# Kernel tuning notes

Measured on AMD Instinct MI355X. Metric: run time of the kernel, lower is better.

Reference implementation:

```python
import jax, jax.numpy as jnp
import numpy as np

L, H, E, FF, B, S = 2, 8, 512, 2048, 8, 1024


def _layernorm(x, g, b, eps=1e-5):
    mu = jnp.mean(x, axis=-1, keepdims=True)
    var = jnp.mean(jnp.square(x - mu), axis=-1, keepdims=True)
    return (x - mu) * jax.lax.rsqrt(var + eps) * g + b


def setup_inputs() -> dict:
    key = jax.random.key(0)
    ks = jax.random.split(key, 16)
    sc = 1.0 / np.sqrt(E)
    d = {
        "x": jax.random.normal(ks[0], (B, S, E), jnp.float32),
        # per-layer, per-head disentangled projections: Linear(E,E) -> weight [out,in]
        "Wq": jax.random.normal(ks[1], (L, H, E, E), jnp.float32) * sc,
        "bq": jnp.zeros((L, H, E), jnp.float32),
        "Wk": jax.random.normal(ks[2], (L, H, E, E), jnp.float32) * sc,
        "bk": jnp.zeros((L, H, E), jnp.float32),
        "Wv": jax.random.normal(ks[3], (L, H, E, E), jnp.float32) * sc,
        "bv": jnp.zeros((L, H, E), jnp.float32),
        "Wo": jax.random.normal(ks[4], (L, H, E, E), jnp.float32) * sc,
        "bo": jnp.zeros((L, H, E), jnp.float32),
        "head_alphas": jax.random.uniform(ks[5], (H,), jnp.float32, 0.5, 1.5),
        "ln1_g": jnp.ones((L, E), jnp.float32),
        "ln1_b": jnp.zeros((L, E), jnp.float32),
        "W1": jax.random.normal(ks[6], (L, FF, E), jnp.float32) * sc,
        "b1": jnp.zeros((L, FF), jnp.float32),
        "W2": jax.random.normal(ks[7], (L, E, FF), jnp.float32) * (1.0 / np.sqrt(FF)),
        "b2": jnp.zeros((L, E), jnp.float32),
        "ln2_g": jnp.ones((L, E), jnp.float32),
        "ln2_b": jnp.zeros((L, E), jnp.float32),
    }
    return d


def reference(x, Wq, bq, Wk, bk, Wv, bv, Wo, bo, head_alphas,
              ln1_g, ln1_b, W1, b1, W2, b2, ln2_g, ln2_b):
    seq = x.shape[1]
    # causal additive mask, as generate_square_subsequent_mask
    causal = jnp.where(jnp.tril(jnp.ones((seq, seq), bool)), 0.0, -jnp.inf).astype(x.dtype)
    scale = jnp.sqrt(jnp.asarray(E, x.dtype))  # head_dim == embed_dim (disentangled)
    ha = head_alphas[None, :, None, None]
    for i in range(L):
        # disentangled per-head projections, batched over heads: [B,H,S,E]
        rq = jnp.einsum('bse,hoe->bhso', x, Wq[i]) + bq[i][None, :, None, :]
        rk = jnp.einsum('bse,hoe->bhso', x, Wk[i]) + bk[i][None, :, None, :]
        rv = jnp.einsum('bse,hoe->bhso', x, Wv[i]) + bv[i][None, :, None, :]
        scores = jnp.einsum('bhqd,bhkd->bhqk', rq, rk) / scale + causal
        attn = jax.nn.softmax(scores, axis=-1)
        ao = jnp.einsum('bhqk,bhkd->bhqd', attn, rv) * ha
        # per-head out_proj then sum over heads
        attn_out = jnp.einsum('bhsd,hod->bso', ao, Wo[i]) + jnp.sum(bo[i], axis=0)
        x = _layernorm(x + attn_out, ln1_g[i], ln1_b[i])
        h = jax.nn.relu(jnp.einsum('bse,fe->bsf', x, W1[i]) + b1[i])
        ff = jnp.einsum('bsf,ef->bse', h, W2[i]) + b2[i]
        x = _layernorm(x + ff, ln2_g[i], ln2_b[i])
    return x
```

## Files before the change

### kernel.cpp

```cpp
#include <hip/hip_runtime.h>
#include <hip/hip_bf16.h>
#include <stdint.h>

#define LL 2
#define HH 8
#define EE 512
#define FFD 2048
#define BB 8
#define SS 1024
#define CB 2
#define NCH (BB / CB)
#define PAIRS (CB * HH)

typedef unsigned short u16;
typedef __attribute__((ext_vector_type(8))) short bf16x8;
typedef __attribute__((ext_vector_type(4))) float f32x4;
typedef __attribute__((ext_vector_type(4))) int int4v;
typedef __attribute__((ext_vector_type(2))) int int2v;

__device__ __forceinline__ u16 f2bf(float f){
  union { float f; unsigned u; } c; c.f = f;
  unsigned r = (c.u + 0x7FFFu + ((c.u >> 16) & 1u)) >> 16;
  return (u16)r;
}

struct GP {
  const u16* A; const u16* B;
  const float* bias; const float* resid;
  void* out;
  long AsMHi, AsMLo, AsH;
  long BsNHi, BsNLo, BsH;
  long Abatch, Bbatch, Obatch, BiasB;
  long OsMHi, OsMLo, OsNHi, OsNLo;
  int M, N, K, causal, Kpart;
  float scale;
};

__device__ __forceinline__ int xcd_swz(int bid, int nwg){
  if (nwg < 16) return bid;
  const int q = nwg >> 3, r = nwg & 7;
  const int xcd = bid & 7, loc = bid >> 3;
  return (xcd < r ? xcd * (q + 1) : r * (q + 1) + (xcd - r) * q) + loc;
}

template<int EP>
__global__ __launch_bounds__(256, 3) void k_gemm(GP p){
  const int tilesN = p.N >> 7;
  const int bid = xcd_swz(blockIdx.x, gridDim.x);
  const int m0 = (bid / tilesN) << 7;
  const int n0 = (bid % tilesN) << 7;
  if (EP == 0 && p.causal && n0 > m0) return;
  const long bb = blockIdx.y;
  const u16* __restrict__ Ag = p.A + bb * p.Abatch;
  const u16* __restrict__ Bg = p.B + bb * p.Bbatch;

  __shared__ __align__(16) u16 As[128 * 64];
  __shared__ __align__(16) u16 Bs[128 * 64];
  char* AsB = (char*)As;
  char* BsB = (char*)Bs;

  const int t = threadIdx.x;
  const int lane = t & 63;
  const int wv = t >> 6;
  const int wr = (wv >> 1) << 6;
  const int wc = (wv & 1) << 6;

  long aoff[4], boff[4];
  #pragma unroll
  for (int j = 0; j < 4; ++j){
    const int r = ((wv << 2) + j) * 8 + (lane >> 3);
    const int kx = ((lane & 7) << 3) ^ ((r & 7) << 3);
    const int gm = m0 + r;
    aoff[j] = (long)(gm >> 10) * p.AsMHi + (long)(gm & 1023) * p.AsMLo + kx;
    const int gn = n0 + r;
    boff[j] = (long)(gn >> 9) * p.BsNHi + (long)(gn & 511) * p.BsNLo + kx;
  }

  int kBeg = 0;
  int Klim = p.K;
  if (EP == 2 && p.causal) { int kl = m0 + 128; Klim = kl < p.K ? kl : p.K; }
  if (EP == 5) { kBeg = (int)bb * p.Kpart; Klim = kBeg + p.Kpart; }

  f32x4 acc[4][4];
  #pragma unroll
  for (int a = 0; a < 4; ++a)
    #pragma unroll
    for (int b = 0; b < 4; ++b)
      acc[a][b] = (f32x4){0.f, 0.f, 0.f, 0.f};

  for (int k0 = kBeg; k0 < Klim; k0 += 64){
    const long ka = (long)(k0 >> 9) * p.AsH + (k0 & 511);
    const long kb = (long)(k0 >> 9) * p.BsH + (k0 & 511);
    __syncthreads();
    #pragma unroll
    for (int j = 0; j < 4; ++j){
      const int ldsOff = (((wv << 2) + j) << 9);
      __builtin_amdgcn_global_load_lds(
          (const __attribute__((address_space(1))) void*)(Ag + aoff[j] + ka),
          (__attribute__((address_space(3))) void*)(As + ldsOff), 16, 0, 0);
      __builtin_amdgcn_global_load_lds(
          (const __attribute__((address_space(1))) void*)(Bg + boff[j] + kb),
          (__attribute__((address_space(3))) void*)(Bs + ldsOff), 16, 0, 0);
    }
    __syncthreads();
    #pragma unroll
    for (int kk = 0; kk < 2; ++kk){
      bf16x8 af[4], bv[4];
      #pragma unroll
      for (int mi = 0; mi < 4; ++mi){
        int row = wr + (mi << 4) + (lane & 15);
        int bc = ((kk << 6) + ((lane >> 4) << 4)) ^ ((row & 7) << 4);
        af[mi] = *reinterpret_cast<const bf16x8*>(AsB + row * 128 + bc);
      }
      #pragma unroll
      for (int ni = 0; ni < 4; ++ni){
        int row = wc + (ni << 4) + (lane & 15);
        int bc = ((kk << 6) + ((lane >> 4) << 4)) ^ ((row & 7) << 4);
        bv[ni] = *reinterpret_cast<const bf16x8*>(BsB + row * 128 + bc);
      }
      #pragma unroll
      for (int mi = 0; mi < 4; ++mi)
        #pragma unroll
        for (int ni = 0; ni < 4; ++ni)
          acc[mi][ni] = __builtin_amdgcn_mfma_f32_16x16x32_bf16(af[mi], bv[ni], acc[mi][ni], 0, 0, 0);
    }
  }

  const int cm = (lane >> 4) << 2;
  const int cn = lane & 15;
  float biasv[4];
  if (EP == 1 || EP == 4){
    #pragma unroll
    for (int ni = 0; ni < 4; ++ni)
      biasv[ni] = p.bias[bb * p.BiasB + n0 + wc + (ni << 4) + cn];
  }
  #pragma unroll
  for (int mi = 0; mi < 4; ++mi){
    #pragma unroll
    for (int i = 0; i < 4; ++i){
      const int m = m0 + wr + (mi << 4) + cm + i;
      const long ob = bb * p.Obatch + (long)(m >> 10) * p.OsMHi + (long)(m & 1023) * p.OsMLo;
      #pragma unroll
      for (int ni = 0; ni < 4; ++ni){
        const int n = n0 + wc + (ni << 4) + cn;
        const long oa = ob + (long)(n >> 9) * p.OsNHi + (long)(n & 511) * p.OsNLo;
        float v = acc[mi][ni][i];
        if (EP == 0) ((u16*)p.out)[oa] = f2bf(v * p.scale);
        else if (EP == 1) ((u16*)p.out)[oa] = f2bf(v + biasv[ni]);
        else if (EP == 2) ((u16*)p.out)[oa] = f2bf(v);
        else if (EP == 5) ((float*)p.out)[oa] = v;
        else { float r = v + biasv[ni]; ((u16*)p.out)[oa] = f2bf(r > 0.f ? r : 0.f); }
      }
    }
  }
}

__global__ __launch_bounds__(128) void k_redln(const float* __restrict__ part,
                                               const float* __restrict__ bias,
                                               const float* __restrict__ resid,
                                               const float* __restrict__ g,
                                               const float* __restrict__ b,
                                               float* __restrict__ fdst,
                                               u16* __restrict__ bdst){
  const long row = blockIdx.x;
  const int t = threadIdx.x;
  const int col = t << 2;
  const long off = row * EE + col;
  const long nX = (long)BB * SS * EE;
  f32x4 s = *reinterpret_cast<const f32x4*>(part + off);
  #pragma unroll
  for (int q = 1; q < 4; ++q){
    f32x4 v = *reinterpret_cast<const f32x4*>(part + q * nX + off);
    s.x += v.x; s.y += v.y; s.z += v.z; s.w += v.w;
  }
  f32x4 bv = *reinterpret_cast<const f32x4*>(bias + col);
  f32x4 rv = *reinterpret_cast<const f32x4*>(resid + off);
  s.x += bv.x + rv.x; s.y += bv.y + rv.y; s.z += bv.z + rv.z; s.w += bv.w + rv.w;

  float ps = s.x + s.y + s.z + s.w;
  #pragma unroll
  for (int o = 32; o; o >>= 1) ps += __shfl_xor(ps, o);
  __shared__ float red[2], red2[2];
  if ((t & 63) == 0) red[t >> 6] = ps;
  __syncthreads();
  const float mean = (red[0] + red[1]) * (1.0f / EE);
  f32x4 d = { s.x - mean, s.y - mean, s.z - mean, s.w - mean };
  float pv = d.x * d.x + d.y * d.y + d.z * d.z + d.w * d.w;
  #pragma unroll
  for (int o = 32; o; o >>= 1) pv += __shfl_xor(pv, o);
  if ((t & 63) == 0) red2[t >> 6] = pv;
  __syncthreads();
  const float var = (red2[0] + red2[1]) * (1.0f / EE);
  const float rstd = rsqrtf(var + 1e-5f);
  f32x4 gv = *reinterpret_cast<const f32x4*>(g + col);
  f32x4 bb = *reinterpret_cast<const f32x4*>(b + col);
  f32x4 o4 = { d.x * rstd * gv.x + bb.x, d.y * rstd * gv.y + bb.y,
               d.z * rstd * gv.z + bb.z, d.w * rstd * gv.w + bb.w };
  *reinterpret_cast<f32x4*>(fdst + off) = o4;
  union { u16 us[4]; int2v v; } u;
  u.us[0] = f2bf(o4.x); u.us[1] = f2bf(o4.y);
  u.us[2] = f2bf(o4.z); u.us[3] = f2bf(o4.w);
  *reinterpret_cast<int2v*>(bdst + off) = u.v;
}

struct SetupP {
  const float *x, *Wq, *Wk, *Wv, *Wo, *W1, *W2, *bq, *bk, *bv, *bo;
  float *xf, *catb, *bos;
  u16 *xb, *wdst;
};
#define SETUP_TA 524288u
#define SETUP_TB 2621440u
#define SETUP_TC 25600u
__global__ __launch_bounds__(256) void k_setup(SetupP sp){
  const unsigned t = blockIdx.x * 256 + threadIdx.x;
  if (t < SETUP_TA){
    const int i = (int)t << 3;
    f32x4 a = *reinterpret_cast<const f32x4*>(sp.x + i);
    f32x4 b = *reinterpret_cast<const f32x4*>(sp.x + i + 4);
    *reinterpret_cast<f32x4*>(sp.xf + i) = a;
    *reinterpret_cast<f32x4*>(sp.xf + i + 4) = b;
    union { u16 us[8]; int4v v; } u;
    #pragma unroll
    for (int j = 0; j < 4; ++j){ u.us[j] = f2bf(a[j]); u.us[4 + j] = f2bf(b[j]); }
    *reinterpret_cast<int4v*>(sp.xb + i) = u.v;
  } else if (t < SETUP_TA + SETUP_TB){
    const size_t j = ((size_t)(t - SETUP_TA)) << 3;
    const size_t R = (size_t)4194304;
    const size_t F = (size_t)2097152;
    const float* src;
    size_t loc;
    if      (j < R)         { src = sp.Wq; loc = j; }
    else if (j < 2*R)       { src = sp.Wk; loc = j - R; }
    else if (j < 3*R)       { src = sp.Wv; loc = j - 2*R; }
    else if (j < 4*R)       { src = sp.Wo; loc = j - 3*R; }
    else if (j < 4*R + F)   { src = sp.W1; loc = j - 4*R; }
    else                    { src = sp.W2; loc = j - 4*R - F; }
    f32x4 a = *reinterpret_cast<const f32x4*>(src + loc);
    f32x4 b = *reinterpret_cast<const f32x4*>(src + loc + 4);
    union { u16 us[8]; int4v v; } u;
    #pragma unroll
    for (int q = 0; q < 4; ++q){ u.us[q] = f2bf(a[q]); u.us[4 + q] = f2bf(b[q]); }
    *reinterpret_cast<int4v*>(sp.wdst + j) = u.v;
  } else {
    const int j = (int)(t - SETUP_TA - SETUP_TB);
    if (j >= 2 * 12800) return;
    const int L = j / 12800;
    const int r = j - L * 12800;
    const int lw = L * HH * EE;
    float* catL = sp.catb + (size_t)L * 3 * HH * EE;
    if (r < 4096) catL[r] = sp.bq[lw + r];
    else if (r < 8192) catL[r] = sp.bk[lw + r - 4096];
    else if (r < 12288) catL[r] = sp.bv[lw + r - 8192];
    else {
      const int o = r - 12288;
      float s = 0.f;
      #pragma unroll
      for (int h = 0; h < HH; ++h) s += sp.bo[lw + h * EE + o];
      sp.bos[L * EE + o] = s;
    }
  }
}

__global__ __launch_bounds__(256) void k_softmax(u16* __restrict__ sp,
                                                 const float* __restrict__ alphas){
  const int wv = threadIdx.x >> 6;
  const long row = (long)blockIdx.x * 4 + wv;
  const int lane = threadIdx.x & 63;
  const int q = (int)(row & (SS - 1));
  const int h = (int)(row >> 10) & (HH - 1);
  const bool half2 = q >= 512;
  u16* rp = sp + row * SS;
  const int i0 = lane << 3;
  float v[8], v2[8];
  float lm = -1e30f;
  {
    bf16x8 a = *reinterpret_cast<const bf16x8*>(rp + i0);
    #pragma unroll
    for (int j = 0; j < 8; ++j){
      union { unsigned u; float f; } c; c.u = ((unsigned)(u16)a[j]) << 16;
      v[j] = (i0 + j <= q) ? c.f : -1e30f;
      lm = fmaxf(lm, v[j]);
    }
  }
  if (half2){
    bf16x8 a = *reinterpret_cast<const bf16x8*>(rp + i0 + 512);
    #pragma unroll
    for (int j = 0; j < 8; ++j){
      union { unsigned u; float f; } c; c.u = ((unsigned)(u16)a[j]) << 16;
      v2[j] = (i0 + 512 + j <= q) ? c.f : -1e30f;
      lm = fmaxf(lm, v2[j]);
    }
  }
  #pragma unroll
  for (int o = 32; o; o >>= 1) lm = fmaxf(lm, __shfl_xor(lm, o));
  float ls = 0.f;
  #pragma unroll
  for (int j = 0; j < 8; ++j){
    float e = exp2f((v[j] - lm) * 1.4426950408889634f);
    e = (i0 + j <= q) ? e : 0.f;
    v[j] = e; ls += e;
  }
  if (half2){
    #pragma unroll
    for (int j = 0; j < 8; ++j){
      float e = exp2f((v2[j] - lm) * 1.4426950408889634f);
      e = (i0 + 512 + j <= q) ? e : 0.f;
      v2[j] = e; ls += e;
    }
  }
  #pragma unroll
  for (int o = 32; o; o >>= 1) ls += __shfl_xor(ls, o);
  const float inv = alphas[h] / ls;
  {
    union { u16 us[8]; bf16x8 v8; } o8;
    #pragma unroll
    for (int j = 0; j < 8; ++j) o8.us[j] = f2bf(v[j] * inv);
    *reinterpret_cast<bf16x8*>(rp + i0) = o8.v8;
  }
  if (half2){
    union { u16 us[8]; bf16x8 v8; } o8;
    #pragma unroll
    for (int j = 0; j < 8; ++j) o8.us[j] = f2bf(v2[j] * inv);
    *reinterpret_cast<bf16x8*>(rp + i0 + 512) = o8.v8;
  }
}

__global__ __launch_bounds__(256) void k_transpose(const u16* __restrict__ v,
                                                   u16* __restrict__ vt){
  const long bh = blockIdx.y;
  const int ts = blockIdx.x >> 3;
  const int td = blockIdx.x & 7;
  const u16* src = v + bh * (long)(SS * EE) + (long)(ts * 64) * EE + td * 64;
  u16* dst = vt + bh * (long)(SS * EE) + (long)(td * 64) * SS + ts * 64;
  __shared__ __align__(16) u16 tl[64][80];
  const int t = threadIdx.x;
  #pragma unroll
  for (int it = 0; it < 2; ++it){
    int id = t + it * 256;
    int r = id >> 3, c = (id & 7) << 3;
    *reinterpret_cast<int4v*>(&tl[r][c]) =
        *reinterpret_cast<const int4v*>(src + (long)r * EE + c);
  }
  __syncthreads();
  #pragma unroll
  for (int it = 0; it < 2; ++it){
    int id = t + it * 256;
    int r = id >> 3, c = (id & 7) << 3;
    union { u16 us[8]; int4v v; } u;
    #pragma unroll
    for (int j = 0; j < 8; ++j) u.us[j] = tl[c + j][r];
    *reinterpret_cast<int4v*>(dst + (long)r * SS + c) = u.v;
  }
}

static inline void gemm_launch(int EP, const GP& p, int batch, hipStream_t st){
  dim3 g((unsigned)((p.M >> 7) * (p.N >> 7)), (unsigned)batch);
  switch (EP){
    case 0: k_gemm<0><<<g, 256, 0, st>>>(p); break;
    case 1: k_gemm<1><<<g, 256, 0, st>>>(p); break;
    case 2: k_gemm<2><<<g, 256, 0, st>>>(p); break;
    case 4: k_gemm<4><<<g, 256, 0, st>>>(p); break;
    case 5: k_gemm<5><<<g, 256, 0, st>>>(p); break;
  }
}

extern "C" void kernel_launch(void* const* d_in, const int* in_sizes, int n_in,
                              void* d_out, int out_size, void* d_ws, size_t ws_size,
                              hipStream_t stream){
  const float* x    = (const float*)d_in[0];
  const float* Wq   = (const float*)d_in[1];
  const float* bq   = (const float*)d_in[2];
  const float* Wk   = (const float*)d_in[3];
  const float* bk   = (const float*)d_in[4];
  const float* Wv   = (const float*)d_in[5];
  const float* bv   = (const float*)d_in[6];
  const float* Wo   = (const float*)d_in[7];
  const float* bo   = (const float*)d_in[8];
  const float* alph = (const float*)d_in[9];
  const float* ln1g = (const float*)d_in[10];
  const float* ln1b = (const float*)d_in[11];
  const float* W1   = (const float*)d_in[12];
  const float* b1   = (const float*)d_in[13];
  const float* W2   = (const float*)d_in[14];
  const float* b2   = (const float*)d_in[15];
  const float* ln2g = (const float*)d_in[16];
  const float* ln2b = (const float*)d_in[17];
  float* out = (float*)d_out;

  const size_t nWh = (size_t)HH * EE * EE;
  const size_t nWf = (size_t)FFD * EE;
  const size_t nX  = (size_t)BB * SS * EE;
  const size_t nQ  = (size_t)BB * HH * SS * EE;
  const size_t nChQ = (size_t)CB * HH * SS * EE;
  const size_t nScC = (size_t)PAIRS * SS * SS;

  char* w = (char*)d_ws;
  size_t off = 0;
  auto take = [&](size_t bytes) -> char* {
    char* p = w + off;
    off += (bytes + 255) & ~(size_t)255;
    return p;
  };

  u16* wqb = (u16*)take(4 * nWh);
  u16* wkb = (u16*)take(4 * nWh);
  u16* wvb = (u16*)take(4 * nWh);
  u16* wob = (u16*)take(4 * nWh);
  u16* w1b = (u16*)take(4 * nWf);
  u16* w2b = (u16*)take(4 * nWf);
  float* xf = (float*)take(4 * nX);
  u16* xb   = (u16*)take(2 * nX);
  u16* ao   = (u16*)take(2 * nQ);
  u16* qc   = (u16*)take(2 * nChQ);
  u16* kc   = (u16*)take(2 * nChQ);
  u16* vc   = (u16*)take(2 * nChQ);
  u16* vtc  = (u16*)take(2 * nChQ);
  u16* sc   = (u16*)take(2 * nScC);
  float* bo_sum  = (float*)take(4 * 2 * EE);
  float* qkvbias = (float*)take(4 * 2 * 3 * HH * EE);
  float* parts = (float*)qc;
  u16* hid = sc;

  SetupP spp{ x, Wq, Wk, Wv, Wo, W1, W2, bq, bk, bv, bo,
              xf, qkvbias, bo_sum, xb, wqb };
  k_setup<<<dim3((SETUP_TA + SETUP_TB + SETUP_TC) / 256), 256, 0, stream>>>(spp);

  for (int i = 0; i < LL; ++i){
    for (int c = 0; c < NCH; ++c){
      GP p{};
      p.AsMHi = (long)1024 * EE; p.AsMLo = EE; p.AsH = 0;
      p.BsNHi = (long)EE * EE;   p.BsNLo = EE; p.BsH = 0;
      p.Abatch = 0; p.Bbatch = (long)(2 * nWh); p.Obatch = (long)nChQ;
      p.BiasB = (long)HH * EE;
      p.OsMHi = (long)HH * SS * EE; p.OsMLo = EE;
      p.OsNHi = (long)SS * EE; p.OsNLo = 1;
      p.M = CB * SS; p.N = HH * EE; p.K = EE;
      p.A = xb + (size_t)c * CB * SS * EE;
      p.B = wqb + (size_t)i * nWh;
      p.bias = qkvbias + (size_t)i * 3 * HH * EE;
      p.out = qc; p.scale = 1.f; p.causal = 0; p.resid = nullptr; p.Kpart = 0;
      gemm_launch(1, p, 3, stream);

      k_transpose<<<dim3(128, PAIRS), 256, 0, stream>>>(vc, vtc);

      GP ps{};
      ps.A = qc; ps.B = kc; ps.out = sc;
      ps.AsMHi = 0; ps.AsMLo = EE; ps.AsH = 0;
      ps.BsNHi = (long)512 * EE; ps.BsNLo = EE; ps.BsH = 0;
      ps.Abatch = (long)SS * EE; ps.Bbatch = (long)SS * EE;
      ps.Obatch = (long)SS * SS; ps.BiasB = 0;
      ps.OsMHi = 0; ps.OsMLo = SS; ps.OsNHi = 512; ps.OsNLo = 1;
      ps.M = SS; ps.N = SS; ps.K = EE;
      ps.scale = 0.044194173824159216f; ps.causal = 1;
      ps.bias = nullptr; ps.resid = nullptr; ps.Kpart = 0;
      gemm_launch(0, ps, PAIRS, stream);

      k_softmax<<<dim3(PAIRS * SS / 4), 256, 0, stream>>>(sc, alph);

      GP pv{};
      pv.A = sc; pv.B = vtc; pv.out = ao + (size_t)c * nChQ;
      pv.AsMHi = 0; pv.AsMLo = SS; pv.AsH = 512;
      pv.BsNHi = 0; pv.BsNLo = SS; pv.BsH = 512;
      pv.Abatch = (long)SS * SS; pv.Bbatch = (long)EE * SS;
      pv.Obatch = (long)SS * EE; pv.BiasB = 0;
      pv.OsMHi = 0; pv.OsMLo = EE; pv.OsNHi = 0; pv.OsNLo = 1;
      pv.M = SS; pv.N = EE; pv.K = SS; pv.causal = 1;
      pv.scale = 1.f; pv.bias = nullptr; pv.resid = nullptr; pv.Kpart = 0;
      gemm_launch(2, pv, PAIRS, stream);
    }

    GP pw{};
    pw.A = ao; pw.B = wob + (size_t)i * nWh; pw.out = parts;
    pw.AsMHi = (long)HH * SS * EE; pw.AsMLo = EE; pw.AsH = (long)SS * EE;
    pw.BsNHi = 0; pw.BsNLo = EE; pw.BsH = (long)EE * EE;
    pw.Abatch = pw.Bbatch = 0; pw.Obatch = (long)nX; pw.BiasB = 0;
    pw.OsMHi = (long)1024 * EE; pw.OsMLo = EE; pw.OsNHi = 0; pw.OsNLo = 1;
    pw.M = BB * SS; pw.N = EE; pw.K = HH * EE; pw.Kpart = (HH * EE) / 4;
    pw.bias = nullptr; pw.resid = nullptr; pw.scale = 1.f; pw.causal = 0;
    gemm_launch(5, pw, 4, stream);
    k_redln<<<dim3(BB * SS), 128, 0, stream>>>(parts, bo_sum + (size_t)i * EE, xf,
                                               ln1g + (size_t)i * EE,
                                               ln1b + (size_t)i * EE, xf, xb);

    GP p1{};
    p1.A = xb; p1.B = w1b + (size_t)i * nWf; p1.out = hid;
    p1.AsMHi = (long)1024 * EE; p1.AsMLo = EE; p1.AsH = 0;
    p1.BsNHi = (long)512 * EE; p1.BsNLo = EE; p1.BsH = 0;
    p1.Abatch = p1.Bbatch = p1.Obatch = 0; p1.BiasB = 0;
    p1.OsMHi = (long)1024 * FFD; p1.OsMLo = FFD; p1.OsNHi = 512; p1.OsNLo = 1;
    p1.M = BB * SS; p1.N = FFD; p1.K = EE;
    p1.bias = b1 + (size_t)i * FFD; p1.resid = nullptr; p1.scale = 1.f;
    p1.causal = 0; p1.Kpart = 0;
    gemm_launch(4, p1, 1, stream);

    GP p2{};
    p2.A = hid; p2.B = w2b + (size_t)i * nWf; p2.out = parts;
    p2.AsMHi = (long)1024 * FFD; p2.AsMLo = FFD; p2.AsH = 512;
    p2.BsNHi = 0; p2.BsNLo = FFD; p2.BsH = 512;
    p2.Abatch = p2.Bbatch = 0; p2.Obatch = (long)nX; p2.BiasB = 0;
    p2.OsMHi = (long)1024 * EE; p2.OsMLo = EE; p2.OsNHi = 0; p2.OsNLo = 1;
    p2.M = BB * SS; p2.N = EE; p2.K = FFD; p2.Kpart = FFD / 4;
    p2.bias = nullptr; p2.resid = nullptr; p2.scale = 1.f; p2.causal = 0;
    gemm_launch(5, p2, 4, stream);
    float* fdst = (i == LL - 1) ? out : xf;
    k_redln<<<dim3(BB * SS), 128, 0, stream>>>(parts, b2 + (size_t)i * EE, xf,
                                               ln2g + (size_t)i * EE,
                                               ln2b + (size_t)i * EE, fdst, xb);
  }
}
```

Before: 1.229 ms.

## Fuse softmax with V transpose, chunk out-projection and LN1, enlarge batch chunks

Softmax and the V transpose become one kernel launch that splits work by block index. The per-head output projection, its split-K reduction and the first layernorm now run inside the batch-chunk loop, writing attention output back into the V buffer, so the full-size attention-output buffer is gone. The batch chunk grows from 2 to 4 sequences. Weight conversion to bf16 moves out of setup into a per-layer kernel, which halves the weight workspace. The aim is fewer launches, a smaller memory footprint and better cache locality, at the cost of more buffer aliasing that must stay correct.

```diff
diff --git a/kernel.cpp b/kernel.cpp
--- a/kernel.cpp
+++ b/kernel.cpp
@@ -8,7 +8,7 @@
 #define FFD 2048
 #define BB 8
 #define SS 1024
-#define CB 2
+#define CB 4
 #define NCH (BB / CB)
 #define PAIRS (CB * HH)
 
@@ -161,16 +161,18 @@
                                                const float* __restrict__ g,
                                                const float* __restrict__ b,
                                                float* __restrict__ fdst,
-                                               u16* __restrict__ bdst){
-  const long row = blockIdx.x;
+                                               u16* __restrict__ bdst,
+                                               long rowBase, long mn){
+  const long lrow = blockIdx.x;
+  const long row = rowBase + lrow;
   const int t = threadIdx.x;
   const int col = t << 2;
+  const long poff = lrow * EE + col;
   const long off = row * EE + col;
-  const long nX = (long)BB * SS * EE;
-  f32x4 s = *reinterpret_cast<const f32x4*>(part + off);
+  f32x4 s = *reinterpret_cast<const f32x4*>(part + poff);
   #pragma unroll
   for (int q = 1; q < 4; ++q){
-    f32x4 v = *reinterpret_cast<const f32x4*>(part + q * nX + off);
+    f32x4 v = *reinterpret_cast<const f32x4*>(part + q * mn + poff);
     s.x += v.x; s.y += v.y; s.z += v.z; s.w += v.w;
   }
   f32x4 bv = *reinterpret_cast<const f32x4*>(bias + col);
@@ -204,12 +206,11 @@
 }
 
 struct SetupP {
-  const float *x, *Wq, *Wk, *Wv, *Wo, *W1, *W2, *bq, *bk, *bv, *bo;
+  const float *x, *bq, *bk, *bv, *bo;
   float *xf, *catb, *bos;
-  u16 *xb, *wdst;
+  u16 *xb;
 };
 #define SETUP_TA 524288u
-#define SETUP_TB 2621440u
 #define SETUP_TC 25600u
 __global__ __launch_bounds__(256) void k_setup(SetupP sp){
   const unsigned t = blockIdx.x * 256 + threadIdx.x;
@@ -223,26 +224,8 @@
     #pragma unroll
     for (int j = 0; j < 4; ++j){ u.us[j] = f2bf(a[j]); u.us[4 + j] = f2bf(b[j]); }
     *reinterpret_cast<int4v*>(sp.xb + i) = u.v;
-  } else if (t < SETUP_TA + SETUP_TB){
-    const size_t j = ((size_t)(t - SETUP_TA)) << 3;
-    const size_t R = (size_t)4194304;
-    const size_t F = (size_t)2097152;
-    const float* src;
-    size_t loc;
-    if      (j < R)         { src = sp.Wq; loc = j; }
-    else if (j < 2*R)       { src = sp.Wk; loc = j - R; }
-    else if (j < 3*R)       { src = sp.Wv; loc = j - 2*R; }
-    else if (j < 4*R)       { src = sp.Wo; loc = j - 3*R; }
-    else if (j < 4*R + F)   { src = sp.W1; loc = j - 4*R; }
-    else                    { src = sp.W2; loc = j - 4*R - F; }
-    f32x4 a = *reinterpret_cast<const f32x4*>(src + loc);
-    f32x4 b = *reinterpret_cast<const f32x4*>(src + loc + 4);
-    union { u16 us[8]; int4v v; } u;
-    #pragma unroll
-    for (int q = 0; q < 4; ++q){ u.us[q] = f2bf(a[q]); u.us[4 + q] = f2bf(b[q]); }
-    *reinterpret_cast<int4v*>(sp.wdst + j) = u.v;
   } else {
-    const int j = (int)(t - SETUP_TA - SETUP_TB);
+    const int j = (int)(t - SETUP_TA);
     if (j >= 2 * 12800) return;
     const int L = j / 12800;
     const int r = j - L * 12800;
@@ -261,95 +244,122 @@
   }
 }
 
-__global__ __launch_bounds__(256) void k_softmax(u16* __restrict__ sp,
-                                                 const float* __restrict__ alphas){
-  const int wv = threadIdx.x >> 6;
-  const long row = (long)blockIdx.x * 4 + wv;
-  const int lane = threadIdx.x & 63;
-  const int q = (int)(row & (SS - 1));
-  const int h = (int)(row >> 10) & (HH - 1);
-  const bool half2 = q >= 512;
-  u16* rp = sp + row * SS;
-  const int i0 = lane << 3;
-  float v[8], v2[8];
-  float lm = -1e30f;
-  {
-    bf16x8 a = *reinterpret_cast<const bf16x8*>(rp + i0);
+struct WcvtP { const float *Wq, *Wk, *Wv, *Wo, *W1, *W2; u16* wdst; };
+#define WCVT_T 1310720u
+__global__ __launch_bounds__(256) void k_wcvt(WcvtP wp){
+  const unsigned t = blockIdx.x * 256 + threadIdx.x;
+  if (t >= WCVT_T) return;
+  const size_t j = ((size_t)t) << 3;
+  const size_t R = (size_t)2097152;
+  const size_t F = (size_t)1048576;
+  const float* src; size_t loc;
+  if      (j < R)       { src = wp.Wq; loc = j; }
+  else if (j < 2*R)     { src = wp.Wk; loc = j - R; }
+  else if (j < 3*R)     { src = wp.Wv; loc = j - 2*R; }
+  else if (j < 4*R)     { src = wp.Wo; loc = j - 3*R; }
+  else if (j < 4*R + F) { src = wp.W1; loc = j - 4*R; }
+  else                  { src = wp.W2; loc = j - 4*R - F; }
+  f32x4 a = *reinterpret_cast<const f32x4*>(src + loc);
+  f32x4 b = *reinterpret_cast<const f32x4*>(src + loc + 4);
+  union { u16 us[8]; int4v v; } u;
+  #pragma unroll
+  for (int q = 0; q < 4; ++q){ u.us[q] = f2bf(a[q]); u.us[4 + q] = f2bf(b[q]); }
+  *reinterpret_cast<int4v*>(wp.wdst + j) = u.v;
+}
+
+#define SM_BLOCKS (PAIRS * SS / 4)
+__global__ __launch_bounds__(256) void k_smt(u16* __restrict__ sp,
+                                             const float* __restrict__ alphas,
+                                             const u16* __restrict__ v,
+                                             u16* __restrict__ vt){
+  if (blockIdx.x < SM_BLOCKS){
+    const int wv = threadIdx.x >> 6;
+    const long row = (long)blockIdx.x * 4 + wv;
+    const int lane = threadIdx.x & 63;
+    const int q = (int)(row & (SS - 1));
+    const int h = (int)(row >> 10) & (HH - 1);
+    const bool half2 = q >= 512;
+    u16* rp = sp + row * SS;
+    const int i0 = lane << 3;
+    float vv[8], v2[8];
+    float lm = -1e30f;
+    {
+      bf16x8 a = *reinterpret_cast<const bf16x8*>(rp + i0);
+      #pragma unroll
+      for (int j = 0; j < 8; ++j){
+        union { unsigned u; float f; } c; c.u = ((unsigned)(u16)a[j]) << 16;
+        vv[j] = (i0 + j <= q) ? c.f : -1e30f;
+        lm = fmaxf(lm, vv[j]);
+      }
+    }
+    if (half2){
+      bf16x8 a = *reinterpret_cast<const bf16x8*>(rp + i0 + 512);
+      #pragma unroll
+      for (int j = 0; j < 8; ++j){
+        union { unsigned u; float f; } c; c.u = ((unsigned)(u16)a[j]) << 16;
+        v2[j] = (i0 + 512 + j <= q) ? c.f : -1e30f;
+        lm = fmaxf(lm, v2[j]);
+      }
+    }
+    #pragma unroll
+    for (int o = 32; o; o >>= 1) lm = fmaxf(lm, __shfl_xor(lm, o));
+    float ls = 0.f;
     #pragma unroll
     for (int j = 0; j < 8; ++j){
-      union { unsigned u; float f; } c; c.u = ((unsigned)(u16)a[j]) << 16;
-      v[j] = (i0 + j <= q) ? c.f : -1e30f;
-      lm = fmaxf(lm, v[j]);
-    }
-  }
-  if (half2){
-    bf16x8 a = *reinterpret_cast<const bf16x8*>(rp + i0 + 512);
-    #pragma unroll
-    for (int j = 0; j < 8; ++j){
-      union { unsigned u; float f; } c; c.u = ((unsigned)(u16)a[j]) << 16;
-      v2[j] = (i0 + 512 + j <= q) ? c.f : -1e30f;
-      lm = fmaxf(lm, v2[j]);
-    }
-  }
-  #pragma unroll
-  for (int o = 32; o; o >>= 1) lm = fmaxf(lm, __shfl_xor(lm, o));
-  float ls = 0.f;
-  #pragma unroll
-  for (int j = 0; j < 8; ++j){
-    float e = exp2f((v[j] - lm) * 1.4426950408889634f);
-    e = (i0 + j <= q) ? e : 0.f;
-    v[j] = e; ls += e;
-  }
-  if (half2){
-    #pragma unroll
-    for (int j = 0; j < 8; ++j){
-      float e = exp2f((v2[j] - lm) * 1.4426950408889634f);
-      e = (i0 + 512 + j <= q) ? e : 0.f;
-      v2[j] = e; ls += e;
-    }
-  }
-  #pragma unroll
-  for (int o = 32; o; o >>= 1) ls += __shfl_xor(ls, o);
-  const float inv = alphas[h] / ls;
-  {
-    union { u16 us[8]; bf16x8 v8; } o8;
-    #pragma unroll
-    for (int j = 0; j < 8; ++j) o8.us[j] = f2bf(v[j] * inv);
-    *reinterpret_cast<bf16x8*>(rp + i0) = o8.v8;
-  }
-  if (half2){
-    union { u16 us[8]; bf16x8 v8; } o8;
-    #pragma unroll
-    for (int j = 0; j < 8; ++j) o8.us[j] = f2bf(v2[j] * inv);
-    *reinterpret_cast<bf16x8*>(rp + i0 + 512) = o8.v8;
-  }
-}
-
-__global__ __launch_bounds__(256) void k_transpose(const u16* __restrict__ v,
-                                                   u16* __restrict__ vt){
-  const long bh = blockIdx.y;
-  const int ts = blockIdx.x >> 3;
-  const int td = blockIdx.x & 7;
-  const u16* src = v + bh * (long)(SS * EE) + (long)(ts * 64) * EE + td * 64;
-  u16* dst = vt + bh * (long)(SS * EE) + (long)(td * 64) * SS + ts * 64;
-  __shared__ __align__(16) u16 tl[64][80];
-  const int t = threadIdx.x;
-  #pragma unroll
-  for (int it = 0; it < 2; ++it){
-    int id = t + it * 256;
-    int r = id >> 3, c = (id & 7) << 3;
-    *reinterpret_cast<int4v*>(&tl[r][c]) =
-        *reinterpret_cast<const int4v*>(src + (long)r * EE + c);
-  }
-  __syncthreads();
-  #pragma unroll
-  for (int it = 0; it < 2; ++it){
-    int id = t + it * 256;
-    int r = id >> 3, c = (id & 7) << 3;
-    union { u16 us[8]; int4v v; } u;
-    #pragma unroll
-    for (int j = 0; j < 8; ++j) u.us[j] = tl[c + j][r];
-    *reinterpret_cast<int4v*>(dst + (long)r * SS + c) = u.v;
+      float e = exp2f((vv[j] - lm) * 1.4426950408889634f);
+      e = (i0 + j <= q) ? e : 0.f;
+      vv[j] = e; ls += e;
+    }
+    if (half2){
+      #pragma unroll
+      for (int j = 0; j < 8; ++j){
+        float e = exp2f((v2[j] - lm) * 1.4426950408889634f);
+        e = (i0 + 512 + j <= q) ? e : 0.f;
+        v2[j] = e; ls += e;
+      }
+    }
+    #pragma unroll
+    for (int o = 32; o; o >>= 1) ls += __shfl_xor(ls, o);
+    const float inv = alphas[h] / ls;
+    {
+      union { u16 us[8]; bf16x8 v8; } o8;
+      #pragma unroll
+      for (int j = 0; j < 8; ++j) o8.us[j] = f2bf(vv[j] * inv);
+      *reinterpret_cast<bf16x8*>(rp + i0) = o8.v8;
+    }
+    if (half2){
+      union { u16 us[8]; bf16x8 v8; } o8;
+      #pragma unroll
+      for (int j = 0; j < 8; ++j) o8.us[j] = f2bf(v2[j] * inv);
+      *reinterpret_cast<bf16x8*>(rp + i0 + 512) = o8.v8;
+    }
+  } else {
+    const int bid2 = blockIdx.x - SM_BLOCKS;
+    const long bh = bid2 >> 7;
+    const int xy = bid2 & 127;
+    const int ts = xy >> 3;
+    const int td = xy & 7;
+    const u16* src = v + bh * (long)(SS * EE) + (long)(ts * 64) * EE + td * 64;
+    u16* dst = vt + bh * (long)(SS * EE) + (long)(td * 64) * SS + ts * 64;
+    __shared__ __align__(16) u16 tl[64][80];
+    const int t = threadIdx.x;
+    #pragma unroll
+    for (int it = 0; it < 2; ++it){
+      int id = t + it * 256;
+      int r = id >> 3, c = (id & 7) << 3;
+      *reinterpret_cast<int4v*>(&tl[r][c]) =
+          *reinterpret_cast<const int4v*>(src + (long)r * EE + c);
+    }
+    __syncthreads();
+    #pragma unroll
+    for (int it = 0; it < 2; ++it){
+      int id = t + it * 256;
+      int r = id >> 3, c = (id & 7) << 3;
+      union { u16 us[8]; int4v v; } u;
+      #pragma unroll
+      for (int j = 0; j < 8; ++j) u.us[j] = tl[c + j][r];
+      *reinterpret_cast<int4v*>(dst + (long)r * SS + c) = u.v;
+    }
   }
 }
 
@@ -390,9 +400,9 @@
   const size_t nWh = (size_t)HH * EE * EE;
   const size_t nWf = (size_t)FFD * EE;
   const size_t nX  = (size_t)BB * SS * EE;
-  const size_t nQ  = (size_t)BB * HH * SS * EE;
   const size_t nChQ = (size_t)CB * HH * SS * EE;
   const size_t nScC = (size_t)PAIRS * SS * SS;
+  const size_t nXc  = (size_t)CB * SS * EE;
 
   char* w = (char*)d_ws;
   size_t off = 0;
@@ -402,15 +412,14 @@
     return p;
   };
 
-  u16* wqb = (u16*)take(4 * nWh);
-  u16* wkb = (u16*)take(4 * nWh);
-  u16* wvb = (u16*)take(4 * nWh);
-  u16* wob = (u16*)take(4 * nWh);
-  u16* w1b = (u16*)take(4 * nWf);
-  u16* w2b = (u16*)take(4 * nWf);
+  u16* wqb = (u16*)take(2 * nWh);
+  u16* wkb = (u16*)take(2 * nWh);
+  u16* wvb = (u16*)take(2 * nWh);
+  u16* wob = (u16*)take(2 * nWh);
+  u16* w1b = (u16*)take(2 * nWf);
+  u16* w2b = (u16*)take(2 * nWf);
   float* xf = (float*)take(4 * nX);
   u16* xb   = (u16*)take(2 * nX);
-  u16* ao   = (u16*)take(2 * nQ);
   u16* qc   = (u16*)take(2 * nChQ);
   u16* kc   = (u16*)take(2 * nChQ);
   u16* vc   = (u16*)take(2 * nChQ);
@@ -418,30 +427,34 @@
   u16* sc   = (u16*)take(2 * nScC);
   float* bo_sum  = (float*)take(4 * 2 * EE);
   float* qkvbias = (float*)take(4 * 2 * 3 * HH * EE);
-  float* parts = (float*)qc;
+  float* partsC = (float*)qc;
+  float* partsF = (float*)qc;
   u16* hid = sc;
 
-  SetupP spp{ x, Wq, Wk, Wv, Wo, W1, W2, bq, bk, bv, bo,
-              xf, qkvbias, bo_sum, xb, wqb };
-  k_setup<<<dim3((SETUP_TA + SETUP_TB + SETUP_TC) / 256), 256, 0, stream>>>(spp);
+  SetupP spp{ x, bq, bk, bv, bo, xf, qkvbias, bo_sum, xb };
+  k_setup<<<dim3((SETUP_TA + SETUP_TC + 255) / 256), 256, 0, stream>>>(spp);
 
   for (int i = 0; i < LL; ++i){
+    WcvtP wp{ Wq + (size_t)i * nWh, Wk + (size_t)i * nWh, Wv + (size_t)i * nWh,
+              Wo + (size_t)i * nWh, W1 + (size_t)i * nWf, W2 + (size_t)i * nWf,
+              wqb };
+    k_wcvt<<<dim3(WCVT_T / 256), 256, 0, stream>>>(wp);
+
     for (int c = 0; c < NCH; ++c){
+      const long rowBase = (long)c * CB * SS;
+
       GP p{};
       p.AsMHi = (long)1024 * EE; p.AsMLo = EE; p.AsH = 0;
       p.BsNHi = (long)EE * EE;   p.BsNLo = EE; p.BsH = 0;
-      p.Abatch = 0; p.Bbatch = (long)(2 * nWh); p.Obatch = (long)nChQ;
+      p.Abatch = 0; p.Bbatch = (long)nWh; p.Obatch = (long)nChQ;
       p.BiasB = (long)HH * EE;
       p.OsMHi = (long)HH * SS * EE; p.OsMLo = EE;
       p.OsNHi = (long)SS * EE; p.OsNLo = 1;
       p.M = CB * SS; p.N = HH * EE; p.K = EE;
-      p.A = xb + (size_t)c * CB * SS * EE;
-      p.B = wqb + (size_t)i * nWh;
-      p.bias = qkvbias + (size_t)i * 3 * HH * EE;
+      p.A = xb + (size_t)rowBase * EE;
+      p.B = wqb; p.bias = qkvbias + (size_t)i * 3 * HH * EE;
       p.out = qc; p.scale = 1.f; p.causal = 0; p.resid = nullptr; p.Kpart = 0;
       gemm_launch(1, p, 3, stream);
-
-      k_transpose<<<dim3(128, PAIRS), 256, 0, stream>>>(vc, vtc);
 
       GP ps{};
       ps.A = qc; ps.B = kc; ps.out = sc;
@@ -455,10 +468,10 @@
       ps.bias = nullptr; ps.resid = nullptr; ps.Kpart = 0;
       gemm_launch(0, ps, PAIRS, stream);
 
-      k_softmax<<<dim3(PAIRS * SS / 4), 256, 0, stream>>>(sc, alph);
+      k_smt<<<dim3(SM_BLOCKS + 128 * PAIRS), 256, 0, stream>>>(sc, alph, vc, vtc);
 
       GP pv{};
-      pv.A = sc; pv.B = vtc; pv.out = ao + (size_t)c * nChQ;
+      pv.A = sc; pv.B = vtc; pv.out = vc;
       pv.AsMHi = 0; pv.AsMLo = SS; pv.AsH = 512;
       pv.BsNHi = 0; pv.BsNLo = SS; pv.BsH = 512;
       pv.Abatch = (long)SS * SS; pv.Bbatch = (long)EE * SS;
@@ -467,23 +480,24 @@
       pv.M = SS; pv.N = EE; pv.K = SS; pv.causal = 1;
       pv.scale = 1.f; pv.bias = nullptr; pv.resid = nullptr; pv.Kpart = 0;
       gemm_launch(2, pv, PAIRS, stream);
-    }
-
-    GP pw{};
-    pw.A = ao; pw.B = wob + (size_t)i * nWh; pw.out = parts;
-    pw.AsMHi = (long)HH * SS * EE; pw.AsMLo = EE; pw.AsH = (long)SS * EE;
-    pw.BsNHi = 0; pw.BsNLo = EE; pw.BsH = (long)EE * EE;
-    pw.Abatch = pw.Bbatch = 0; pw.Obatch = (long)nX; pw.BiasB = 0;
-    pw.OsMHi = (long)1024 * EE; pw.OsMLo = EE; pw.OsNHi = 0; pw.OsNLo = 1;
-    pw.M = BB * SS; pw.N = EE; pw.K = HH * EE; pw.Kpart = (HH * EE) / 4;
-    pw.bias = nullptr; pw.resid = nullptr; pw.scale = 1.f; pw.causal = 0;
-    gemm_launch(5, pw, 4, stream);
-    k_redln<<<dim3(BB * SS), 128, 0, stream>>>(parts, bo_sum + (size_t)i * EE, xf,
-                                               ln1g + (size_t)i * EE,
-                                               ln1b + (size_t)i * EE, xf, xb);
+
+      GP pw{};
+      pw.A = vc; pw.B = wob; pw.out = partsC;
+      pw.AsMHi = (long)HH * SS * EE; pw.AsMLo = EE; pw.AsH = (long)SS * EE;
+      pw.BsNHi = 0; pw.BsNLo = EE; pw.BsH = (long)EE * EE;
+      pw.Abatch = pw.Bbatch = 0; pw.Obatch = (long)nXc; pw.BiasB = 0;
+      pw.OsMHi = (long)1024 * EE; pw.OsMLo = EE; pw.OsNHi = 0; pw.OsNLo = 1;
+      pw.M = CB * SS; pw.N = EE; pw.K = HH * EE; pw.Kpart = (HH * EE) / 4;
+      pw.bias = nullptr; pw.resid = nullptr; pw.scale = 1.f; pw.causal = 0;
+      gemm_launch(5, pw, 4, stream);
+      k_redln<<<dim3(CB * SS), 128, 0, stream>>>(partsC, bo_sum + (size_t)i * EE,
+                                                 xf, ln1g + (size_t)i * EE,
+                                                 ln1b + (size_t)i * EE, xf, xb,
+                                                 rowBase, (long)nXc);
+    }
 
     GP p1{};
-    p1.A = xb; p1.B = w1b + (size_t)i * nWf; p1.out = hid;
+    p1.A = xb; p1.B = w1b; p1.out = hid;
     p1.AsMHi = (long)1024 * EE; p1.AsMLo = EE; p1.AsH = 0;
     p1.BsNHi = (long)512 * EE; p1.BsNLo = EE; p1.BsH = 0;
     p1.Abatch = p1.Bbatch = p1.Obatch = 0; p1.BiasB = 0;
@@ -494,7 +508,7 @@
     gemm_launch(4, p1, 1, stream);
 
     GP p2{};
-    p2.A = hid; p2.B = w2b + (size_t)i * nWf; p2.out = parts;
+    p2.A = hid; p2.B = w2b; p2.out = partsF;
     p2.AsMHi = (long)1024 * FFD; p2.AsMLo = FFD; p2.AsH = 512;
     p2.BsNHi = 0; p2.BsNLo = FFD; p2.BsH = 512;
     p2.Abatch = p2.Bbatch = 0; p2.Obatch = (long)nX; p2.BiasB = 0;
@@ -503,8 +517,9 @@
     p2.bias = nullptr; p2.resid = nullptr; p2.scale = 1.f; p2.causal = 0;
     gemm_launch(5, p2, 4, stream);
     float* fdst = (i == LL - 1) ? out : xf;
-    k_redln<<<dim3(BB * SS), 128, 0, stream>>>(parts, b2 + (size_t)i * EE, xf,
+    k_redln<<<dim3(BB * SS), 128, 0, stream>>>(partsF, b2 + (size_t)i * EE, xf,
                                                ln2g + (size_t)i * EE,
-                                               ln2b + (size_t)i * EE, fdst, xb);
-  }
-}
+                                               ln2b + (size_t)i * EE, fdst, xb,
+                                               0, (long)nX);
+  }
+}
```

After: 1.122 ms, median of 2. 1.1x faster.
